# Performance work log

Hardware: AMD Instinct MI355X
Metric: run time of the kernel (lower is better)

The kernel has to match this reference:

```python
import jax, jax.numpy as jnp
import numpy as np
from jax import lax

B, S, F = 64, 63, 64          # batch, window length, num_past_features
T, NF, OUT = 12, 63, 1        # pred_sequence_length, forecast feats, output_size
C, K = 32, 3                  # hidden channels, kernel size
DILS = (1, 2, 4, 8, 16)       # S = (K-1)*sum(DILS)+1 = 63 -> conv stack reduces to length 1


def setup_inputs() -> dict:
    key = jax.random.key(0)
    ks = jax.random.split(key, 8)
    sc = 0.1
    x = jax.random.normal(ks[0], (B, S, F), dtype=jnp.float32)
    x_forecasts = jax.random.normal(ks[1], (B, T, NF), dtype=jnp.float32)
    # per-feature conv stacks stored as grouped-conv weights (feature_group_count=F)
    w0 = jax.random.normal(ks[2], (F * C, 1, K), dtype=jnp.float32) * sc
    b0 = jnp.zeros((F * C,), dtype=jnp.float32)
    wmid = jax.random.normal(ks[3], (3, F * C, C, K), dtype=jnp.float32) * sc
    bmid = jnp.zeros((3, F * C), dtype=jnp.float32)
    wlast = jax.random.normal(ks[4], (F * 1, C, K), dtype=jnp.float32) * sc
    blast = jnp.zeros((F,), dtype=jnp.float32)
    linW = jax.random.normal(ks[5], (OUT, F + NF), dtype=jnp.float32) * sc
    linb = jnp.zeros((OUT,), dtype=jnp.float32)
    return dict(x=x, x_forecasts=x_forecasts, w0=w0, b0=b0, wmid=wmid,
                bmid=bmid, wlast=wlast, blast=blast, linW=linW, linb=linb)


def _dconv(h, w, d):
    # h: [B, F*Cin, L]; grouped dilated conv, one group per past feature
    return lax.conv_general_dilated(h, w, window_strides=(1,), padding='VALID',
                                    rhs_dilation=(d,),
                                    dimension_numbers=('NCH', 'OIH', 'NCH'),
                                    feature_group_count=F)


def _step(xw, xf, w0, b0, wmid, bmid, wlast, blast, linW, linb):
    # xw: [B, S, F] window; xf: [B, NF] forecast features for this step
    h = jnp.transpose(xw, (0, 2, 1))                       # [B, F, S]
    h = jax.nn.relu(_dconv(h, w0, DILS[0]) + b0[None, :, None])
    for k in range(3):
        h = jax.nn.relu(_dconv(h, wmid[k], DILS[k + 1]) + bmid[k][None, :, None])
    h = _dconv(h, wlast, DILS[4]) + blast[None, :, None]   # [B, F, 1], no final relu
    feat = jnp.concatenate([h[:, :, 0], xf], axis=1)       # [B, F+NF]
    return feat @ linW.T + linb                            # [B, OUT]


def reference(x, x_forecasts, w0, b0, wmid, bmid, wlast, blast, linW, linb):
    params = (w0, b0, wmid, bmid, wlast, blast, linW, linb)
    out0 = _step(x, x_forecasts[:, 0], *params)

    def body(carry, xs):
        xw, prev = carry
        xf_i, xf_ip1 = xs
        add = jnp.concatenate([xf_i, prev], axis=1)[:, None, :]   # [B,1,F] since NF+OUT=F
        xw = jnp.concatenate([xw[:, 1:, :], add], axis=1)          # slide window
        out = _step(xw, xf_ip1, *params)
        return (xw, out), out

    xs = (jnp.swapaxes(x_forecasts[:, :-1], 0, 1),   # [T-1, B, NF]
          jnp.swapaxes(x_forecasts[:, 1:], 0, 1))
    _, outs = lax.scan(body, (x, out0), xs)          # [T-1, B, OUT]
    return jnp.swapaxes(jnp.concatenate([out0[None], outs], axis=0), 0, 1)  # [B, T, OUT]
```

## Files before the change

### kernel.cpp

```cpp
#include <hip/hip_runtime.h>


typedef _Float16 f16;
typedef _Float16 h2 __attribute__((ext_vector_type(2)));
typedef _Float16 f16x4 __attribute__((ext_vector_type(4)));
typedef _Float16 f16x8 __attribute__((ext_vector_type(8)));
typedef float f32x16 __attribute__((ext_vector_type(16)));

#define OFF_H4    0
#define OFF_ST    49152
#define ST_L0     0
#define ST_L1     128
#define ST_L2     384
#define ST_L3     896
#define ST_STRIDE 1760
#define OFF_H40   161792
#define OFF_RECH  161856
#define OFF_PRM   166464
#define OFF_XFT   167488

#define RECH_N 9216
#define TAIL_N 59392

#define RPAD 36
#define NROW 100

__device__ __forceinline__ void stage_wrow(
    const float* __restrict__ wmid, int m, int f, int tid, f16* wrow)
{
  const float* src = wmid + m * 196608 + f * 3072 + tid * 12;
  f16* dst = wrow + (tid >> 3) * 100 + (tid & 7) * 12;
#pragma unroll
  for (int u = 0; u < 3; ++u) {
    const float4 v = *reinterpret_cast<const float4*>(src + u * 4);
    dst[u * 4 + 0] = (f16)v.x; dst[u * 4 + 1] = (f16)v.y;
    dst[u * 4 + 2] = (f16)v.z; dst[u * 4 + 3] = (f16)v.w;
  }
}

__device__ __forceinline__ void mfma_tile2(
    const f16* IN, f16* OUT, int d, int base,
    const f16* __restrict__ wrow, int lane, const float* sBias)
{
  const int lg = lane >> 5;
  const int co = lane & 31;
  const int col = base + co;

  f16x8 afr[6];
#pragma unroll
  for (int h = 0; h < 2; ++h) {
    const f16* wp = wrow + co * 100 + (h * 16 + lg * 8) * 3;
    f16x4 w4[6];
#pragma unroll
    for (int u = 0; u < 6; ++u) w4[u] = *(const f16x4*)(wp + u * 4);
#pragma unroll
    for (int t = 0; t < 3; ++t)
#pragma unroll
      for (int j = 0; j < 8; ++j) {
        const int o = 3 * j + t;
        afr[t * 2 + h][j] = w4[o >> 2][o & 3];
      }
  }

  f32x16 acc;
#pragma unroll
  for (int r = 0; r < 16; ++r)
    acc[r] = sBias[(r & 3) + 8 * (r >> 2) + 4 * lg];

#pragma unroll
  for (int t = 0; t < 3; ++t) {
#pragma unroll
    for (int h = 0; h < 2; ++h) {
      const f16* bp = IN + (col + t * d) * RPAD + h * 16 + lg * 8;
      f16x4 lo = *(const f16x4*)bp;
      f16x4 hi = *(const f16x4*)(bp + 4);
      f16x8 b = __builtin_shufflevector(lo, hi, 0, 1, 2, 3, 4, 5, 6, 7);
      acc = __builtin_amdgcn_mfma_f32_32x32x16_f16(afr[t * 2 + h], b, acc, 0, 0, 0);
    }
  }

#pragma unroll
  for (int q = 0; q < 4; ++q) {
    const int co0 = q * 8 + 4 * lg;
    f16x4 w;
#pragma unroll
    for (int e = 0; e < 4; ++e)
      w[e] = (f16)fmaxf(acc[q * 4 + e], 0.f);
    *(f16x4*)(OUT + col * RPAD + co0) = w;
  }
}

__global__ __launch_bounds__(256) void tcn_pre(
    const float* __restrict__ x, const float* __restrict__ xfc,
    const float* __restrict__ w0, const float* __restrict__ b0,
    const float* __restrict__ wmid, const float* __restrict__ bmid,
    const float* __restrict__ wlast, const float* __restrict__ blast,
    const float* __restrict__ linW, const float* __restrict__ linb,
    float* __restrict__ ws)
{
  const int blk = blockIdx.x;
  const int tid = threadIdx.x;

  if (blk >= 4096) {
    const int idx = (blk - 4096) * 256 + tid;
    if (idx < RECH_N) {
      const int e = idx & 7, lane = (idx >> 3) & 63, q = idx >> 9;
      const int i = q * 8 + e;
      const int m = i / 48, r2 = i % 48;
      const int k = r2 >> 4, ci = r2 & 15;
      const int c = lane & 31, cib = (lane >> 5) * 16;
      ((f16*)(ws + OFF_RECH))[idx] =
          (f16)wmid[m * 196608 + (2016 + c) * 96 + (cib + ci) * 3 + k];
    } else if (idx < RECH_N + 1024) {
      const int r = idx - RECH_N;
      const int e = r & 3, lane = (r >> 2) & 63, q = r >> 8;
      const int i = q * 4 + e;
      const int c = lane & 31;
      float v = 0.f;
      if (i < 3)        v = w0[(2016 + c) * 3 + i];
      else if (i == 3)  v = b0[2016 + c];
      else if (i < 7)   v = bmid[(i - 4) * 2048 + 2016 + c];
      else if (i < 10)  v = wlast[63 * 96 + c * 3 + (i - 7)];
      else if (i == 10) v = blast[63];
      else if (i == 11) v = linW[63];
      else if (i == 12) v = linb[0];
      ws[OFF_PRM + r] = v;
    } else if (idx < TAIL_N) {
      const int r = idx - (RECH_N + 1024);
      const int b = r / 768, rem = r % 768;
      const int q = rem >> 8, lane = (rem >> 2) & 63, e = rem & 3;
      const int i = q * 4 + e;
      ws[OFF_XFT + r] = (lane < 63 && i < 12) ? xfc[(b * 12 + i) * 63 + lane] : 0.f;
    }
    return;
  }

  const int b = blk >> 6;
  const int f = blk & 63;
  const bool lastf = (f == 63);
  const int lane = tid & 63;
  const int g = __builtin_amdgcn_readfirstlane(tid >> 6);

  __shared__ float sIn[80];
  __shared__ float sBias[3][32];
  __shared__ f16 actA[NROW * RPAD];
  __shared__ f16 actB[NROW * RPAD];
  __shared__ __align__(8) f16 wrow[32 * 100];

  for (int t = tid; t < 80; t += 256) {
    float v = 0.f;
    if (t < 63)                 v = x[(b * 63 + t) * 64 + f];
    else if (t < 74 && !lastf)  v = xfc[(b * 12 + (t - 63)) * 63 + f];
    sIn[t] = v;
  }
  if (tid < 96) sBias[tid >> 5][tid & 31] = bmid[(tid >> 5) * 2048 + f * 32 + (tid & 31)];
  for (int i = tid; i < (NROW - 72) * RPAD; i += 256) actA[72 * RPAD + i] = (f16)0.f;
  for (int i = tid; i < (NROW - 68) * RPAD; i += 256) actB[68 * RPAD + i] = (f16)0.f;
  stage_wrow(wmid, 0, f, tid, wrow);
  __syncthreads();

  {
    const float* wb  = w0 + (f * 32 + g * 8) * 3;
    const float* bbp = b0 + f * 32 + g * 8;
#pragma unroll
    for (int it = 0; it < 2; ++it) {
      const int p = lane + it * 64;
      if (p < 72) {
        const float i0 = sIn[p], i1 = sIn[p + 1], i2 = sIn[p + 2];
        f16x4 wv[2];
#pragma unroll
        for (int j = 0; j < 8; ++j) {
          float v = fmaf(wb[j * 3 + 0], i0,
                    fmaf(wb[j * 3 + 1], i1,
                    fmaf(wb[j * 3 + 2], i2, bbp[j])));
          wv[j >> 2][j & 3] = (f16)fmaxf(v, 0.f);
        }
        *(f16x4*)(actA + p * RPAD + g * 8)     = wv[0];
        *(f16x4*)(actA + p * RPAD + g * 8 + 4) = wv[1];
      }
    }
  }
  __syncthreads();

  float* st = ws + OFF_ST + b * ST_STRIDE;

  if (lastf) {
    for (int t = tid; t < 128; t += 256)
      st[ST_L0 + t] = (float)actA[(57 + (t >> 5)) * RPAD + (t & 31)];
  }
  if (g < 3) mfma_tile2(actA, actB, 2, g * 32, wrow, lane, sBias[0]);
  __syncthreads();

  stage_wrow(wmid, 1, f, tid, wrow);
  if (lastf) {
    for (int t = tid; t < 256; t += 256)
      st[ST_L1 + t] = (float)actB[(49 + (t >> 5)) * RPAD + (t & 31)];
  }
  __syncthreads();

  if (g < 2) mfma_tile2(actB, actA, 4, g * 32, wrow, lane, sBias[1]);
  __syncthreads();

  stage_wrow(wmid, 2, f, tid, wrow);
  if (lastf) {
    for (int t = tid; t < 512; t += 256)
      st[ST_L2 + t] = (float)actA[(33 + (t >> 5)) * RPAD + (t & 31)];
  }
  __syncthreads();

  if (g < 2) mfma_tile2(actA, actB, 8, g * 32, wrow, lane, sBias[2]);
  __syncthreads();

  if (lastf) {
    for (int t = tid; t < 864; t += 256)
      st[ST_L3 + t] = (float)actB[(1 + (t >> 5)) * RPAD + (t & 31)];
  }
  if (tid < 12) {
    const int p = tid;
    float acc = blast[f];
    const float* wl = wlast + f * 96;
#pragma unroll
    for (int k = 0; k < 3; ++k) {
      const int row = p + 16 * k;
#pragma unroll
      for (int ci0 = 0; ci0 < 32; ci0 += 4) {
        f16x4 av = *(const f16x4*)(actB + row * RPAD + ci0);
#pragma unroll
        for (int e = 0; e < 4; ++e)
          acc = fmaf(wl[(ci0 + e) * 3 + k], (float)av[e], acc);
      }
    }
    if (!lastf) {
      ws[OFF_H4 + b * 768 + (p >> 2) * 256 + f * 4 + (p & 3)] = acc;
    } else {
      ws[OFF_H4 + b * 768 + (p >> 2) * 256 + 63 * 4 + (p & 3)] = 0.f;
      if (p == 0) ws[OFF_H40 + b] = acc;
    }
  }
}


__device__ __forceinline__ float fd2(h2 a, h2 b, float c) {
#if __has_builtin(__builtin_amdgcn_fdot2)
  return __builtin_amdgcn_fdot2(a, b, c, false);
#else
  return fmaf((float)a[0], (float)b[0], fmaf((float)a[1], (float)b[1], c));
#endif
}

__device__ __forceinline__ float dotv(f16x8 w, f16x8 a, float acc) {
  h2 w0 = {w[0], w[1]}, a0 = {a[0], a[1]};
  h2 w1 = {w[2], w[3]}, a1 = {a[2], a[3]};
  h2 w2 = {w[4], w[5]}, a2 = {a[4], a[5]};
  h2 w3 = {w[6], w[7]}, a3 = {a[6], a[7]};
  acc = fd2(w0, a0, acc);
  acc = fd2(w1, a1, acc);
  acc = fd2(w2, a2, acc);
  acc = fd2(w3, a3, acc);
  return acc;
}

__device__ __forceinline__ f16x8 combineh(f16x8 lo, f16x8 hi) {
  f16x8 s = lo + hi;
#pragma unroll
  for (int i = 0; i < 8; ++i) s[i] = (s[i] > (f16)0.f) ? s[i] : (f16)0.f;
  return s;
}

__device__ __forceinline__ void load16f(const float* p, float* r) {
  const float4* q = reinterpret_cast<const float4*>(p);
  const float4 v0 = q[0], v1 = q[1], v2 = q[2], v3 = q[3];
  r[0]=v0.x;  r[1]=v0.y;  r[2]=v0.z;  r[3]=v0.w;
  r[4]=v1.x;  r[5]=v1.y;  r[6]=v1.z;  r[7]=v1.w;
  r[8]=v2.x;  r[9]=v2.y;  r[10]=v2.z; r[11]=v2.w;
  r[12]=v3.x; r[13]=v3.y; r[14]=v3.z; r[15]=v3.w;
}

__global__ __launch_bounds__(64, 1) void tcn_seq(
    const float* __restrict__ x,
    const float* __restrict__ linW,
    const float* __restrict__ ws, float* __restrict__ out)
{
  const int b = blockIdx.x;
  const int tid = threadIdx.x;
  const int c = tid & 31;
  const int h = tid >> 5;
  const int cib = h * 16;

  __shared__ __align__(16) f16 L0h[15 * 32];
  __shared__ __align__(16) f16 L1p[2][19 * 32];
  __shared__ __align__(16) f16 L2p[2][27 * 32];
  __shared__ __align__(16) f16 wseqh[18 * 64 * 8];
  __shared__ __align__(16) float qs[32];
  __shared__ float preArr[12];

  const float* stp = ws + OFF_ST + b * ST_STRIDE;

  for (int t = tid; t < 128; t += 64) L0h[t] = (f16)stp[ST_L0 + t];
  for (int t = tid; t < 256; t += 64) { L1p[0][t] = (f16)stp[ST_L1 + t]; L1p[1][t] = (f16)0.f; }
  for (int t = tid; t < 512; t += 64) { L2p[0][t] = (f16)stp[ST_L2 + t]; L2p[1][t] = (f16)0.f; }

  {
    const f16* rech = (const f16*)(ws + OFF_RECH);
#pragma unroll
    for (int q = 0; q < 18; ++q)
      *(f16x8*)(wseqh + (q * 64 + tid) * 8) = *(const f16x8*)(rech + (q * 64 + tid) * 8);
  }

  float prm[16];
  {
    const float* tab = ws + OFF_PRM;
#pragma unroll
    for (int q = 0; q < 4; ++q) {
      const float4 v = *reinterpret_cast<const float4*>(tab + (q * 64 + tid) * 4);
      prm[q * 4 + 0] = v.x; prm[q * 4 + 1] = v.y;
      prm[q * 4 + 2] = v.z; prm[q * 4 + 3] = v.w;
    }
  }
  const float w00 = prm[0],  w01 = prm[1],  w02 = prm[2],  b00 = prm[3];
  const float bm0 = prm[4],  bm1 = prm[5],  bm2 = prm[6];
  const float wl0c = prm[7], wl1c = prm[8], wl2c = prm[9];
  const float bl = prm[10],  lw63 = prm[11], lb0 = prm[12];

  const float xv61 = x[(b * 63 + 61) * 64 + 63];
  const float xv62 = x[(b * 63 + 62) * 64 + 63];
  const float h40v = ws[OFF_H40 + b];

  float accv[12];
  {
    float lw = 0.f, lwx = 0.f;
    if (tid < 63) { lw = linW[tid]; lwx = linW[64 + tid]; }
    float h4v[12], xv[12];
#pragma unroll
    for (int q = 0; q < 3; ++q) {
      const float4 hv  = *reinterpret_cast<const float4*>(ws + OFF_H4 + b * 768 + q * 256 + tid * 4);
      const float4 xvv = *reinterpret_cast<const float4*>(ws + OFF_XFT + b * 768 + q * 256 + tid * 4);
      h4v[q*4+0] = hv.x; h4v[q*4+1] = hv.y; h4v[q*4+2] = hv.z; h4v[q*4+3] = hv.w;
      xv[q*4+0] = xvv.x; xv[q*4+1] = xvv.y; xv[q*4+2] = xvv.z; xv[q*4+3] = xvv.w;
    }
#pragma unroll
    for (int i = 0; i < 12; ++i) accv[i] = fmaf(lw, h4v[i], lwx * xv[i]);

    if (tid < 32) {
#pragma unroll
      for (int i = 1; i < 12; ++i) {
        const float qc = fmaf(wl0c, stp[ST_L3 + (i - 1) * 32 + tid],
                              wl1c * stp[ST_L3 + (i + 15) * 32 + tid]);
        accv[i] = fmaf(lw63, qc, accv[i]);
      }
    }
#pragma unroll
    for (int r = 1; r < 64; r <<= 1) {
#pragma unroll
      for (int i = 0; i < 12; ++i) accv[i] += __shfl_xor(accv[i], r);
    }
  }
  if (tid == 0) {
#pragma unroll
    for (int i = 1; i < 12; ++i) preArr[i] = accv[i] + lb0 + lw63 * bl;
  }
  __syncthreads();

  const f16* wbase = wseqh;
  asm volatile("" : "+v"(wbase));

  const float out0 = fmaf(lw63, h40v, accv[0] + lb0);
  if (tid == 0) out[b * 12 + 0] = out0;
  float o1 = out0, o2 = xv62, o3 = xv61;

#pragma unroll 1
  for (int s = 1; s < 12; ++s) {
    const float preS = preArr[s];

    const float nL0 = fmaxf(fmaf(w00, o3, fmaf(w01, o2, fmaf(w02, o1, b00))), 0.f);
    L0h[(3 + s) * 32 + c] = (f16)nL0;

    float v1;
    {
      const f16* wp = wbase + (0 * 6 * 64 + tid) * 8;
      f16x8 W0 = *(const f16x8*)(wp);
      f16x8 W1 = *(const f16x8*)(wp + 64 * 8);
      f16x8 W2 = *(const f16x8*)(wp + 2 * 64 * 8);
      f16x8 W3 = *(const f16x8*)(wp + 3 * 64 * 8);
      f16x8 W4 = *(const f16x8*)(wp + 4 * 64 * 8);
      f16x8 W5 = *(const f16x8*)(wp + 5 * 64 * 8);
      const f16* r0p = L0h + (s - 1) * 32 + cib;
      const f16* r1p = L0h + (s + 1) * 32 + cib;
      const f16* np  = L0h + (3 + s) * 32 + cib;
      f16x8 R0a = *(const f16x8*)r0p, R0b = *(const f16x8*)(r0p + 8);
      f16x8 R1a = *(const f16x8*)r1p, R1b = *(const f16x8*)(r1p + 8);
      f16x8 Na  = *(const f16x8*)np,  Nb  = *(const f16x8*)(np + 8);
      float a0 = dotv(W0, R0a, 0.f), a1 = dotv(W1, R0b, 0.f);
      a0 = dotv(W2, R1a, a0);        a1 = dotv(W3, R1b, a1);
      a0 = dotv(W4, Na, a0);         a1 = dotv(W5, Nb, a1);
      v1 = a0 + a1 + (h == 0 ? bm0 : 0.f);
    }
    L1p[h][(7 + s) * 32 + c] = (f16)v1;

    float v2;
    {
      const f16* wp = wbase + (1 * 6 * 64 + tid) * 8;
      f16x8 W0 = *(const f16x8*)(wp);
      f16x8 W1 = *(const f16x8*)(wp + 64 * 8);
      f16x8 W2 = *(const f16x8*)(wp + 2 * 64 * 8);
      f16x8 W3 = *(const f16x8*)(wp + 3 * 64 * 8);
      f16x8 W4 = *(const f16x8*)(wp + 4 * 64 * 8);
      f16x8 W5 = *(const f16x8*)(wp + 5 * 64 * 8);
      const int i0 = (s - 1) * 32 + cib, i1 = (s + 3) * 32 + cib, in = (7 + s) * 32 + cib;
      f16x8 R0a = combineh(*(const f16x8*)(&L1p[0][i0]),     *(const f16x8*)(&L1p[1][i0]));
      f16x8 R0b = combineh(*(const f16x8*)(&L1p[0][i0 + 8]), *(const f16x8*)(&L1p[1][i0 + 8]));
      f16x8 R1a = combineh(*(const f16x8*)(&L1p[0][i1]),     *(const f16x8*)(&L1p[1][i1]));
      f16x8 R1b = combineh(*(const f16x8*)(&L1p[0][i1 + 8]), *(const f16x8*)(&L1p[1][i1 + 8]));
      f16x8 Na  = combineh(*(const f16x8*)(&L1p[0][in]),     *(const f16x8*)(&L1p[1][in]));
      f16x8 Nb  = combineh(*(const f16x8*)(&L1p[0][in + 8]), *(const f16x8*)(&L1p[1][in + 8]));
      float a0 = dotv(W0, R0a, 0.f), a1 = dotv(W1, R0b, 0.f);
      a0 = dotv(W2, R1a, a0);        a1 = dotv(W3, R1b, a1);
      a0 = dotv(W4, Na, a0);         a1 = dotv(W5, Nb, a1);
      v2 = a0 + a1 + (h == 0 ? bm1 : 0.f);
    }
    L2p[h][(15 + s) * 32 + c] = (f16)v2;

    float v3;
    {
      const f16* wp = wbase + (2 * 6 * 64 + tid) * 8;
      f16x8 W0 = *(const f16x8*)(wp);
      f16x8 W1 = *(const f16x8*)(wp + 64 * 8);
      f16x8 W2 = *(const f16x8*)(wp + 2 * 64 * 8);
      f16x8 W3 = *(const f16x8*)(wp + 3 * 64 * 8);
      f16x8 W4 = *(const f16x8*)(wp + 4 * 64 * 8);
      f16x8 W5 = *(const f16x8*)(wp + 5 * 64 * 8);
      const int i0 = (s - 1) * 32 + cib, i1 = (s + 7) * 32 + cib, in = (15 + s) * 32 + cib;
      f16x8 R0a = combineh(*(const f16x8*)(&L2p[0][i0]),     *(const f16x8*)(&L2p[1][i0]));
      f16x8 R0b = combineh(*(const f16x8*)(&L2p[0][i0 + 8]), *(const f16x8*)(&L2p[1][i0 + 8]));
      f16x8 R1a = combineh(*(const f16x8*)(&L2p[0][i1]),     *(const f16x8*)(&L2p[1][i1]));
      f16x8 R1b = combineh(*(const f16x8*)(&L2p[0][i1 + 8]), *(const f16x8*)(&L2p[1][i1 + 8]));
      f16x8 Na  = combineh(*(const f16x8*)(&L2p[0][in]),     *(const f16x8*)(&L2p[1][in]));
      f16x8 Nb  = combineh(*(const f16x8*)(&L2p[0][in + 8]), *(const f16x8*)(&L2p[1][in + 8]));
      float a0 = dotv(W0, R0a, 0.f), a1 = dotv(W1, R0b, 0.f);
      a0 = dotv(W2, R1a, a0);        a1 = dotv(W3, R1b, a1);
      a0 = dotv(W4, Na, a0);         a1 = dotv(W5, Nb, a1);
      v3 = a0 + a1 + (h == 0 ? bm2 : 0.f);
    }
    v3 += __shfl_xor(v3, 32);
    const float nL3 = fmaxf(v3, 0.f);

    if (h == 0) qs[c] = wl2c * nL3;
    float qa[16], qb[16];
    load16f(qs, qa); load16f(qs + 16, qb);
    float s0 = 0.f, s1 = 0.f, s2 = 0.f, s3 = 0.f;
#pragma unroll
    for (int i = 0; i < 16; i += 4) {
      s0 += qa[i + 0] + qb[i + 0];
      s1 += qa[i + 1] + qb[i + 1];
      s2 += qa[i + 2] + qb[i + 2];
      s3 += qa[i + 3] + qb[i + 3];
    }
    const float S = (s0 + s1) + (s2 + s3);
    const float outs = fmaf(lw63, S, preS);
    if (tid == 0) out[b * 12 + s] = outs;
    o3 = o2; o2 = o1; o1 = outs;
  }
}


extern "C" void kernel_launch(void* const* d_in, const int* in_sizes, int n_in,
                              void* d_out, int out_size, void* d_ws, size_t ws_size,
                              hipStream_t stream) {
  const float* x     = (const float*)d_in[0];
  const float* xfc   = (const float*)d_in[1];
  const float* w0    = (const float*)d_in[2];
  const float* b0    = (const float*)d_in[3];
  const float* wmid  = (const float*)d_in[4];
  const float* bmid  = (const float*)d_in[5];
  const float* wlast = (const float*)d_in[6];
  const float* blast = (const float*)d_in[7];
  const float* linW  = (const float*)d_in[8];
  const float* linb  = (const float*)d_in[9];
  float* out = (float*)d_out;
  float* ws  = (float*)d_ws;

  tcn_pre<<<4096 + 232, 256, 0, stream>>>(
      x, xfc, w0, b0, wmid, bmid, wlast, blast, linW, linb, ws);
  tcn_seq<<<64, 64, 0, stream>>>(x, linW, ws, out);
}
```

Baseline: 41.85 us.

## Fuse pre and sequential kernels into one launch with atomic-counter handoff

Merges the parallel conv-stack kernel and the per-batch sequential kernel into a single launch. The trailing 64 blocks spin on global atomic counters until all compute and tail-prep blocks have finished, then run the recurrent steps. They also prefetch the reshaped weights as soon as the tail counter completes. This removes one kernel launch and the gap between launches, but adds a memset and relies on all earlier blocks being scheduled before the spinning blocks, which risks deadlock if they are not.

```diff
diff --git a/kernel.cpp b/kernel.cpp
--- a/kernel.cpp
+++ b/kernel.cpp
@@ -18,12 +18,24 @@
 #define OFF_RECH  161856
 #define OFF_PRM   166464
 #define OFF_XFT   167488
+#define OFF_CTR   216640
 
 #define RECH_N 9216
 #define TAIL_N 59392
+#define NCOMP  4096
+#define NTAIL  232
+#define NSEQ   64
 
 #define RPAD 36
 #define NROW 100
+
+#if __has_builtin(__builtin_amdgcn_fence)
+#define ACQ_FENCE() __builtin_amdgcn_fence(__ATOMIC_ACQUIRE, "agent")
+#else
+#define ACQ_FENCE() __threadfence()
+#endif
+
+#define SMEM_BYTES 25472
 
 __device__ __forceinline__ void stage_wrow(
     const float* __restrict__ wmid, int m, int f, int tid, f16* wrow)
@@ -90,19 +102,250 @@
   }
 }
 
-__global__ __launch_bounds__(256) void tcn_pre(
+__device__ __forceinline__ float fd2(h2 a, h2 b, float c) {
+#if __has_builtin(__builtin_amdgcn_fdot2)
+  return __builtin_amdgcn_fdot2(a, b, c, false);
+#else
+  return fmaf((float)a[0], (float)b[0], fmaf((float)a[1], (float)b[1], c));
+#endif
+}
+
+__device__ __forceinline__ float dotv(f16x8 w, f16x8 a, float acc) {
+  h2 w0 = {w[0], w[1]}, a0 = {a[0], a[1]};
+  h2 w1 = {w[2], w[3]}, a1 = {a[2], a[3]};
+  h2 w2 = {w[4], w[5]}, a2 = {a[4], a[5]};
+  h2 w3 = {w[6], w[7]}, a3 = {a[6], a[7]};
+  acc = fd2(w0, a0, acc);
+  acc = fd2(w1, a1, acc);
+  acc = fd2(w2, a2, acc);
+  acc = fd2(w3, a3, acc);
+  return acc;
+}
+
+__device__ __forceinline__ f16x8 combineh(f16x8 lo, f16x8 hi) {
+  f16x8 s = lo + hi;
+#pragma unroll
+  for (int i = 0; i < 8; ++i) s[i] = (s[i] > (f16)0.f) ? s[i] : (f16)0.f;
+  return s;
+}
+
+__device__ __forceinline__ void load16f(const float* p, float* r) {
+  const float4* q = reinterpret_cast<const float4*>(p);
+  const float4 v0 = q[0], v1 = q[1], v2 = q[2], v3 = q[3];
+  r[0]=v0.x;  r[1]=v0.y;  r[2]=v0.z;  r[3]=v0.w;
+  r[4]=v1.x;  r[5]=v1.y;  r[6]=v1.z;  r[7]=v1.w;
+  r[8]=v2.x;  r[9]=v2.y;  r[10]=v2.z; r[11]=v2.w;
+  r[12]=v3.x; r[13]=v3.y; r[14]=v3.z; r[15]=v3.w;
+}
+
+__global__ __launch_bounds__(256) void tcn_all(
     const float* __restrict__ x, const float* __restrict__ xfc,
     const float* __restrict__ w0, const float* __restrict__ b0,
     const float* __restrict__ wmid, const float* __restrict__ bmid,
     const float* __restrict__ wlast, const float* __restrict__ blast,
     const float* __restrict__ linW, const float* __restrict__ linb,
-    float* __restrict__ ws)
+    float* __restrict__ ws, float* __restrict__ out)
 {
+  __shared__ __align__(16) char smem[SMEM_BYTES];
   const int blk = blockIdx.x;
   const int tid = threadIdx.x;
-
-  if (blk >= 4096) {
-    const int idx = (blk - 4096) * 256 + tid;
+  int* ctr = (int*)(ws + OFF_CTR);
+
+  if (blk >= NCOMP + NTAIL) {
+    if (tid >= 64) return;
+    const int b = blk - (NCOMP + NTAIL);
+    const int c = tid & 31;
+    const int h = tid >> 5;
+    const int cib = h * 16;
+
+    f16* wseqh = (f16*)smem;
+    f16* L0h   = (f16*)(smem + 18432);
+    f16* L1p0  = (f16*)(smem + 19392);
+    f16* L1p1  = (f16*)(smem + 20608);
+    f16* L2p0  = (f16*)(smem + 21824);
+    f16* L2p1  = (f16*)(smem + 23552);
+    float* qs     = (float*)(smem + 25280);
+    float* preArr = (float*)(smem + 25408);
+
+    const float xv61 = x[(b * 63 + 61) * 64 + 63];
+    const float xv62 = x[(b * 63 + 62) * 64 + 63];
+    float lw = 0.f, lwx = 0.f;
+    if (tid < 63) { lw = linW[tid]; lwx = linW[64 + tid]; }
+
+    while (__hip_atomic_load(&ctr[1], __ATOMIC_RELAXED, __HIP_MEMORY_SCOPE_AGENT) < NTAIL)
+      __builtin_amdgcn_s_sleep(4);
+    ACQ_FENCE();
+
+    {
+      const f16* rech = (const f16*)(ws + OFF_RECH);
+#pragma unroll
+      for (int q = 0; q < 18; ++q)
+        *(f16x8*)(wseqh + (q * 64 + tid) * 8) = *(const f16x8*)(rech + (q * 64 + tid) * 8);
+    }
+    float prm[16];
+    {
+      const float* tab = ws + OFF_PRM;
+#pragma unroll
+      for (int q = 0; q < 4; ++q) {
+        const float4 v = *reinterpret_cast<const float4*>(tab + (q * 64 + tid) * 4);
+        prm[q * 4 + 0] = v.x; prm[q * 4 + 1] = v.y;
+        prm[q * 4 + 2] = v.z; prm[q * 4 + 3] = v.w;
+      }
+    }
+    float xv[12];
+#pragma unroll
+    for (int q = 0; q < 3; ++q) {
+      const float4 vv = *reinterpret_cast<const float4*>(ws + OFF_XFT + b * 768 + q * 256 + tid * 4);
+      xv[q*4+0] = vv.x; xv[q*4+1] = vv.y; xv[q*4+2] = vv.z; xv[q*4+3] = vv.w;
+    }
+    const float w00 = prm[0],  w01 = prm[1],  w02 = prm[2],  b00 = prm[3];
+    const float bm0 = prm[4],  bm1 = prm[5],  bm2 = prm[6];
+    const float wl0c = prm[7], wl1c = prm[8], wl2c = prm[9];
+    const float bl = prm[10],  lw63 = prm[11], lb0 = prm[12];
+
+    while (__hip_atomic_load(&ctr[0], __ATOMIC_RELAXED, __HIP_MEMORY_SCOPE_AGENT) < NCOMP)
+      __builtin_amdgcn_s_sleep(4);
+    ACQ_FENCE();
+
+    const float* stp = ws + OFF_ST + b * ST_STRIDE;
+    for (int t = tid; t < 128; t += 64) L0h[t] = (f16)stp[ST_L0 + t];
+    for (int t = tid; t < 256; t += 64) { L1p0[t] = (f16)stp[ST_L1 + t]; L1p1[t] = (f16)0.f; }
+    for (int t = tid; t < 512; t += 64) { L2p0[t] = (f16)stp[ST_L2 + t]; L2p1[t] = (f16)0.f; }
+    const float h40v = ws[OFF_H40 + b];
+
+    float accv[12];
+    {
+      float h4v[12];
+#pragma unroll
+      for (int q = 0; q < 3; ++q) {
+        const float4 hv = *reinterpret_cast<const float4*>(ws + OFF_H4 + b * 768 + q * 256 + tid * 4);
+        h4v[q*4+0] = hv.x; h4v[q*4+1] = hv.y; h4v[q*4+2] = hv.z; h4v[q*4+3] = hv.w;
+      }
+#pragma unroll
+      for (int i = 0; i < 12; ++i) accv[i] = fmaf(lw, h4v[i], lwx * xv[i]);
+      if (tid < 32) {
+#pragma unroll
+        for (int i = 1; i < 12; ++i) {
+          const float qc = fmaf(wl0c, stp[ST_L3 + (i - 1) * 32 + tid],
+                                wl1c * stp[ST_L3 + (i + 15) * 32 + tid]);
+          accv[i] = fmaf(lw63, qc, accv[i]);
+        }
+      }
+#pragma unroll
+      for (int r = 1; r < 64; r <<= 1) {
+#pragma unroll
+        for (int i = 0; i < 12; ++i) accv[i] += __shfl_xor(accv[i], r);
+      }
+    }
+    if (tid == 0) {
+#pragma unroll
+      for (int i = 1; i < 12; ++i) preArr[i] = accv[i] + lb0 + lw63 * bl;
+    }
+
+    const f16* wbase = wseqh;
+    asm volatile("" : "+v"(wbase));
+
+    const float out0 = fmaf(lw63, h40v, accv[0] + lb0);
+    if (tid == 0) out[b * 12 + 0] = out0;
+    float o1 = out0, o2 = xv62, o3 = xv61;
+
+#pragma unroll 1
+    for (int s = 1; s < 12; ++s) {
+      const float preS = preArr[s];
+
+      const float nL0 = fmaxf(fmaf(w00, o3, fmaf(w01, o2, fmaf(w02, o1, b00))), 0.f);
+      L0h[(3 + s) * 32 + c] = (f16)nL0;
+
+      float v1;
+      {
+        const f16* wp = wbase + (0 * 6 * 64 + tid) * 8;
+        f16x8 W0 = *(const f16x8*)(wp);
+        f16x8 W1 = *(const f16x8*)(wp + 64 * 8);
+        f16x8 W2 = *(const f16x8*)(wp + 2 * 64 * 8);
+        f16x8 W3 = *(const f16x8*)(wp + 3 * 64 * 8);
+        f16x8 W4 = *(const f16x8*)(wp + 4 * 64 * 8);
+        f16x8 W5 = *(const f16x8*)(wp + 5 * 64 * 8);
+        const f16* r0p = L0h + (s - 1) * 32 + cib;
+        const f16* r1p = L0h + (s + 1) * 32 + cib;
+        const f16* np  = L0h + (3 + s) * 32 + cib;
+        f16x8 R0a = *(const f16x8*)r0p, R0b = *(const f16x8*)(r0p + 8);
+        f16x8 R1a = *(const f16x8*)r1p, R1b = *(const f16x8*)(r1p + 8);
+        f16x8 Na  = *(const f16x8*)np,  Nb  = *(const f16x8*)(np + 8);
+        float a0 = dotv(W0, R0a, 0.f), a1 = dotv(W1, R0b, 0.f);
+        a0 = dotv(W2, R1a, a0);        a1 = dotv(W3, R1b, a1);
+        a0 = dotv(W4, Na, a0);         a1 = dotv(W5, Nb, a1);
+        v1 = a0 + a1 + (h == 0 ? bm0 : 0.f);
+      }
+      (h ? L1p1 : L1p0)[(7 + s) * 32 + c] = (f16)v1;
+
+      float v2;
+      {
+        const f16* wp = wbase + (1 * 6 * 64 + tid) * 8;
+        f16x8 W0 = *(const f16x8*)(wp);
+        f16x8 W1 = *(const f16x8*)(wp + 64 * 8);
+        f16x8 W2 = *(const f16x8*)(wp + 2 * 64 * 8);
+        f16x8 W3 = *(const f16x8*)(wp + 3 * 64 * 8);
+        f16x8 W4 = *(const f16x8*)(wp + 4 * 64 * 8);
+        f16x8 W5 = *(const f16x8*)(wp + 5 * 64 * 8);
+        const int i0 = (s - 1) * 32 + cib, i1 = (s + 3) * 32 + cib, in = (7 + s) * 32 + cib;
+        f16x8 R0a = combineh(*(const f16x8*)(L1p0 + i0),     *(const f16x8*)(L1p1 + i0));
+        f16x8 R0b = combineh(*(const f16x8*)(L1p0 + i0 + 8), *(const f16x8*)(L1p1 + i0 + 8));
+        f16x8 R1a = combineh(*(const f16x8*)(L1p0 + i1),     *(const f16x8*)(L1p1 + i1));
+        f16x8 R1b = combineh(*(const f16x8*)(L1p0 + i1 + 8), *(const f16x8*)(L1p1 + i1 + 8));
+        f16x8 Na  = combineh(*(const f16x8*)(L1p0 + in),     *(const f16x8*)(L1p1 + in));
+        f16x8 Nb  = combineh(*(const f16x8*)(L1p0 + in + 8), *(const f16x8*)(L1p1 + in + 8));
+        float a0 = dotv(W0, R0a, 0.f), a1 = dotv(W1, R0b, 0.f);
+        a0 = dotv(W2, R1a, a0);        a1 = dotv(W3, R1b, a1);
+        a0 = dotv(W4, Na, a0);         a1 = dotv(W5, Nb, a1);
+        v2 = a0 + a1 + (h == 0 ? bm1 : 0.f);
+      }
+      (h ? L2p1 : L2p0)[(15 + s) * 32 + c] = (f16)v2;
+
+      float v3;
+      {
+        const f16* wp = wbase + (2 * 6 * 64 + tid) * 8;
+        f16x8 W0 = *(const f16x8*)(wp);
+        f16x8 W1 = *(const f16x8*)(wp + 64 * 8);
+        f16x8 W2 = *(const f16x8*)(wp + 2 * 64 * 8);
+        f16x8 W3 = *(const f16x8*)(wp + 3 * 64 * 8);
+        f16x8 W4 = *(const f16x8*)(wp + 4 * 64 * 8);
+        f16x8 W5 = *(const f16x8*)(wp + 5 * 64 * 8);
+        const int i0 = (s - 1) * 32 + cib, i1 = (s + 7) * 32 + cib, in = (15 + s) * 32 + cib;
+        f16x8 R0a = combineh(*(const f16x8*)(L2p0 + i0),     *(const f16x8*)(L2p1 + i0));
+        f16x8 R0b = combineh(*(const f16x8*)(L2p0 + i0 + 8), *(const f16x8*)(L2p1 + i0 + 8));
+        f16x8 R1a = combineh(*(const f16x8*)(L2p0 + i1),     *(const f16x8*)(L2p1 + i1));
+        f16x8 R1b = combineh(*(const f16x8*)(L2p0 + i1 + 8), *(const f16x8*)(L2p1 + i1 + 8));
+        f16x8 Na  = combineh(*(const f16x8*)(L2p0 + in),     *(const f16x8*)(L2p1 + in));
+        f16x8 Nb  = combineh(*(const f16x8*)(L2p0 + in + 8), *(const f16x8*)(L2p1 + in + 8));
+        float a0 = dotv(W0, R0a, 0.f), a1 = dotv(W1, R0b, 0.f);
+        a0 = dotv(W2, R1a, a0);        a1 = dotv(W3, R1b, a1);
+        a0 = dotv(W4, Na, a0);         a1 = dotv(W5, Nb, a1);
+        v3 = a0 + a1 + (h == 0 ? bm2 : 0.f);
+      }
+      v3 += __shfl_xor(v3, 32);
+      const float nL3 = fmaxf(v3, 0.f);
+
+      if (h == 0) qs[c] = wl2c * nL3;
+      float qa[16], qb[16];
+      load16f(qs, qa); load16f(qs + 16, qb);
+      float s0 = 0.f, s1 = 0.f, s2 = 0.f, s3 = 0.f;
+#pragma unroll
+      for (int i = 0; i < 16; i += 4) {
+        s0 += qa[i + 0] + qb[i + 0];
+        s1 += qa[i + 1] + qb[i + 1];
+        s2 += qa[i + 2] + qb[i + 2];
+        s3 += qa[i + 3] + qb[i + 3];
+      }
+      const float S = (s0 + s1) + (s2 + s3);
+      const float outs = fmaf(lw63, S, preS);
+      if (tid == 0) out[b * 12 + s] = outs;
+      o3 = o2; o2 = o1; o1 = outs;
+    }
+    return;
+  }
+
+  if (blk >= NCOMP) {
+    const int idx = (blk - NCOMP) * 256 + tid;
     if (idx < RECH_N) {
       const int e = idx & 7, lane = (idx >> 3) & 63, q = idx >> 9;
       const int i = q * 8 + e;
@@ -125,13 +368,15 @@
       else if (i == 11) v = linW[63];
       else if (i == 12) v = linb[0];
       ws[OFF_PRM + r] = v;
-    } else if (idx < TAIL_N) {
+    } else {
       const int r = idx - (RECH_N + 1024);
       const int b = r / 768, rem = r % 768;
       const int q = rem >> 8, lane = (rem >> 2) & 63, e = rem & 3;
       const int i = q * 4 + e;
       ws[OFF_XFT + r] = (lane < 63 && i < 12) ? xfc[(b * 12 + i) * 63 + lane] : 0.f;
     }
+    __syncthreads();
+    if (tid == 0) { __threadfence(); atomicAdd(&ctr[1], 1); }
     return;
   }
 
@@ -141,11 +386,11 @@
   const int lane = tid & 63;
   const int g = __builtin_amdgcn_readfirstlane(tid >> 6);
 
-  __shared__ float sIn[80];
-  __shared__ float sBias[3][32];
-  __shared__ f16 actA[NROW * RPAD];
-  __shared__ f16 actB[NROW * RPAD];
-  __shared__ __align__(8) f16 wrow[32 * 100];
+  float* sIn   = (float*)smem;
+  float* sBias = (float*)(smem + 320);
+  f16*   actA  = (f16*)(smem + 704);
+  f16*   actB  = (f16*)(smem + 7904);
+  f16*   wrow  = (f16*)(smem + 15104);
 
   for (int t = tid; t < 80; t += 256) {
     float v = 0.f;
@@ -153,7 +398,7 @@
     else if (t < 74 && !lastf)  v = xfc[(b * 12 + (t - 63)) * 63 + f];
     sIn[t] = v;
   }
-  if (tid < 96) sBias[tid >> 5][tid & 31] = bmid[(tid >> 5) * 2048 + f * 32 + (tid & 31)];
+  if (tid < 96) sBias[(tid >> 5) * 32 + (tid & 31)] = bmid[(tid >> 5) * 2048 + f * 32 + (tid & 31)];
   for (int i = tid; i < (NROW - 72) * RPAD; i += 256) actA[72 * RPAD + i] = (f16)0.f;
   for (int i = tid; i < (NROW - 68) * RPAD; i += 256) actB[68 * RPAD + i] = (f16)0.f;
   stage_wrow(wmid, 0, f, tid, wrow);
@@ -188,7 +433,7 @@
     for (int t = tid; t < 128; t += 256)
       st[ST_L0 + t] = (float)actA[(57 + (t >> 5)) * RPAD + (t & 31)];
   }
-  if (g < 3) mfma_tile2(actA, actB, 2, g * 32, wrow, lane, sBias[0]);
+  if (g < 3) mfma_tile2(actA, actB, 2, g * 32, wrow, lane, sBias + 0);
   __syncthreads();
 
   stage_wrow(wmid, 1, f, tid, wrow);
@@ -198,7 +443,7 @@
   }
   __syncthreads();
 
-  if (g < 2) mfma_tile2(actB, actA, 4, g * 32, wrow, lane, sBias[1]);
+  if (g < 2) mfma_tile2(actB, actA, 4, g * 32, wrow, lane, sBias + 32);
   __syncthreads();
 
   stage_wrow(wmid, 2, f, tid, wrow);
@@ -208,7 +453,7 @@
   }
   __syncthreads();
 
-  if (g < 2) mfma_tile2(actA, actB, 8, g * 32, wrow, lane, sBias[2]);
+  if (g < 2) mfma_tile2(actA, actB, 8, g * 32, wrow, lane, sBias + 64);
   __syncthreads();
 
   if (lastf) {
@@ -237,229 +482,8 @@
       if (p == 0) ws[OFF_H40 + b] = acc;
     }
   }
-}
-
-
-__device__ __forceinline__ float fd2(h2 a, h2 b, float c) {
-#if __has_builtin(__builtin_amdgcn_fdot2)
-  return __builtin_amdgcn_fdot2(a, b, c, false);
-#else
-  return fmaf((float)a[0], (float)b[0], fmaf((float)a[1], (float)b[1], c));
-#endif
-}
-
-__device__ __forceinline__ float dotv(f16x8 w, f16x8 a, float acc) {
-  h2 w0 = {w[0], w[1]}, a0 = {a[0], a[1]};
-  h2 w1 = {w[2], w[3]}, a1 = {a[2], a[3]};
-  h2 w2 = {w[4], w[5]}, a2 = {a[4], a[5]};
-  h2 w3 = {w[6], w[7]}, a3 = {a[6], a[7]};
-  acc = fd2(w0, a0, acc);
-  acc = fd2(w1, a1, acc);
-  acc = fd2(w2, a2, acc);
-  acc = fd2(w3, a3, acc);
-  return acc;
-}
-
-__device__ __forceinline__ f16x8 combineh(f16x8 lo, f16x8 hi) {
-  f16x8 s = lo + hi;
-#pragma unroll
-  for (int i = 0; i < 8; ++i) s[i] = (s[i] > (f16)0.f) ? s[i] : (f16)0.f;
-  return s;
-}
-
-__device__ __forceinline__ void load16f(const float* p, float* r) {
-  const float4* q = reinterpret_cast<const float4*>(p);
-  const float4 v0 = q[0], v1 = q[1], v2 = q[2], v3 = q[3];
-  r[0]=v0.x;  r[1]=v0.y;  r[2]=v0.z;  r[3]=v0.w;
-  r[4]=v1.x;  r[5]=v1.y;  r[6]=v1.z;  r[7]=v1.w;
-  r[8]=v2.x;  r[9]=v2.y;  r[10]=v2.z; r[11]=v2.w;
-  r[12]=v3.x; r[13]=v3.y; r[14]=v3.z; r[15]=v3.w;
-}
-
-__global__ __launch_bounds__(64, 1) void tcn_seq(
-    const float* __restrict__ x,
-    const float* __restrict__ linW,
-    const float* __restrict__ ws, float* __restrict__ out)
-{
-  const int b = blockIdx.x;
-  const int tid = threadIdx.x;
-  const int c = tid & 31;
-  const int h = tid >> 5;
-  const int cib = h * 16;
-
-  __shared__ __align__(16) f16 L0h[15 * 32];
-  __shared__ __align__(16) f16 L1p[2][19 * 32];
-  __shared__ __align__(16) f16 L2p[2][27 * 32];
-  __shared__ __align__(16) f16 wseqh[18 * 64 * 8];
-  __shared__ __align__(16) float qs[32];
-  __shared__ float preArr[12];
-
-  const float* stp = ws + OFF_ST + b * ST_STRIDE;
-
-  for (int t = tid; t < 128; t += 64) L0h[t] = (f16)stp[ST_L0 + t];
-  for (int t = tid; t < 256; t += 64) { L1p[0][t] = (f16)stp[ST_L1 + t]; L1p[1][t] = (f16)0.f; }
-  for (int t = tid; t < 512; t += 64) { L2p[0][t] = (f16)stp[ST_L2 + t]; L2p[1][t] = (f16)0.f; }
-
-  {
-    const f16* rech = (const f16*)(ws + OFF_RECH);
-#pragma unroll
-    for (int q = 0; q < 18; ++q)
-      *(f16x8*)(wseqh + (q * 64 + tid) * 8) = *(const f16x8*)(rech + (q * 64 + tid) * 8);
-  }
-
-  float prm[16];
-  {
-    const float* tab = ws + OFF_PRM;
-#pragma unroll
-    for (int q = 0; q < 4; ++q) {
-      const float4 v = *reinterpret_cast<const float4*>(tab + (q * 64 + tid) * 4);
-      prm[q * 4 + 0] = v.x; prm[q * 4 + 1] = v.y;
-      prm[q * 4 + 2] = v.z; prm[q * 4 + 3] = v.w;
-    }
-  }
-  const float w00 = prm[0],  w01 = prm[1],  w02 = prm[2],  b00 = prm[3];
-  const float bm0 = prm[4],  bm1 = prm[5],  bm2 = prm[6];
-  const float wl0c = prm[7], wl1c = prm[8], wl2c = prm[9];
-  const float bl = prm[10],  lw63 = prm[11], lb0 = prm[12];
-
-  const float xv61 = x[(b * 63 + 61) * 64 + 63];
-  const float xv62 = x[(b * 63 + 62) * 64 + 63];
-  const float h40v = ws[OFF_H40 + b];
-
-  float accv[12];
-  {
-    float lw = 0.f, lwx = 0.f;
-    if (tid < 63) { lw = linW[tid]; lwx = linW[64 + tid]; }
-    float h4v[12], xv[12];
-#pragma unroll
-    for (int q = 0; q < 3; ++q) {
-      const float4 hv  = *reinterpret_cast<const float4*>(ws + OFF_H4 + b * 768 + q * 256 + tid * 4);
-      const float4 xvv = *reinterpret_cast<const float4*>(ws + OFF_XFT + b * 768 + q * 256 + tid * 4);
-      h4v[q*4+0] = hv.x; h4v[q*4+1] = hv.y; h4v[q*4+2] = hv.z; h4v[q*4+3] = hv.w;
-      xv[q*4+0] = xvv.x; xv[q*4+1] = xvv.y; xv[q*4+2] = xvv.z; xv[q*4+3] = xvv.w;
-    }
-#pragma unroll
-    for (int i = 0; i < 12; ++i) accv[i] = fmaf(lw, h4v[i], lwx * xv[i]);
-
-    if (tid < 32) {
-#pragma unroll
-      for (int i = 1; i < 12; ++i) {
-        const float qc = fmaf(wl0c, stp[ST_L3 + (i - 1) * 32 + tid],
-                              wl1c * stp[ST_L3 + (i + 15) * 32 + tid]);
-        accv[i] = fmaf(lw63, qc, accv[i]);
-      }
-    }
-#pragma unroll
-    for (int r = 1; r < 64; r <<= 1) {
-#pragma unroll
-      for (int i = 0; i < 12; ++i) accv[i] += __shfl_xor(accv[i], r);
-    }
-  }
-  if (tid == 0) {
-#pragma unroll
-    for (int i = 1; i < 12; ++i) preArr[i] = accv[i] + lb0 + lw63 * bl;
-  }
-  __syncthreads();
-
-  const f16* wbase = wseqh;
-  asm volatile("" : "+v"(wbase));
-
-  const float out0 = fmaf(lw63, h40v, accv[0] + lb0);
-  if (tid == 0) out[b * 12 + 0] = out0;
-  float o1 = out0, o2 = xv62, o3 = xv61;
-
-#pragma unroll 1
-  for (int s = 1; s < 12; ++s) {
-    const float preS = preArr[s];
-
-    const float nL0 = fmaxf(fmaf(w00, o3, fmaf(w01, o2, fmaf(w02, o1, b00))), 0.f);
-    L0h[(3 + s) * 32 + c] = (f16)nL0;
-
-    float v1;
-    {
-      const f16* wp = wbase + (0 * 6 * 64 + tid) * 8;
-      f16x8 W0 = *(const f16x8*)(wp);
-      f16x8 W1 = *(const f16x8*)(wp + 64 * 8);
-      f16x8 W2 = *(const f16x8*)(wp + 2 * 64 * 8);
-      f16x8 W3 = *(const f16x8*)(wp + 3 * 64 * 8);
-      f16x8 W4 = *(const f16x8*)(wp + 4 * 64 * 8);
-      f16x8 W5 = *(const f16x8*)(wp + 5 * 64 * 8);
-      const f16* r0p = L0h + (s - 1) * 32 + cib;
-      const f16* r1p = L0h + (s + 1) * 32 + cib;
-      const f16* np  = L0h + (3 + s) * 32 + cib;
-      f16x8 R0a = *(const f16x8*)r0p, R0b = *(const f16x8*)(r0p + 8);
-      f16x8 R1a = *(const f16x8*)r1p, R1b = *(const f16x8*)(r1p + 8);
-      f16x8 Na  = *(const f16x8*)np,  Nb  = *(const f16x8*)(np + 8);
-      float a0 = dotv(W0, R0a, 0.f), a1 = dotv(W1, R0b, 0.f);
-      a0 = dotv(W2, R1a, a0);        a1 = dotv(W3, R1b, a1);
-      a0 = dotv(W4, Na, a0);         a1 = dotv(W5, Nb, a1);
-      v1 = a0 + a1 + (h == 0 ? bm0 : 0.f);
-    }
-    L1p[h][(7 + s) * 32 + c] = (f16)v1;
-
-    float v2;
-    {
-      const f16* wp = wbase + (1 * 6 * 64 + tid) * 8;
-      f16x8 W0 = *(const f16x8*)(wp);
-      f16x8 W1 = *(const f16x8*)(wp + 64 * 8);
-      f16x8 W2 = *(const f16x8*)(wp + 2 * 64 * 8);
-      f16x8 W3 = *(const f16x8*)(wp + 3 * 64 * 8);
-      f16x8 W4 = *(const f16x8*)(wp + 4 * 64 * 8);
-      f16x8 W5 = *(const f16x8*)(wp + 5 * 64 * 8);
-      const int i0 = (s - 1) * 32 + cib, i1 = (s + 3) * 32 + cib, in = (7 + s) * 32 + cib;
-      f16x8 R0a = combineh(*(const f16x8*)(&L1p[0][i0]),     *(const f16x8*)(&L1p[1][i0]));
-      f16x8 R0b = combineh(*(const f16x8*)(&L1p[0][i0 + 8]), *(const f16x8*)(&L1p[1][i0 + 8]));
-      f16x8 R1a = combineh(*(const f16x8*)(&L1p[0][i1]),     *(const f16x8*)(&L1p[1][i1]));
-      f16x8 R1b = combineh(*(const f16x8*)(&L1p[0][i1 + 8]), *(const f16x8*)(&L1p[1][i1 + 8]));
-      f16x8 Na  = combineh(*(const f16x8*)(&L1p[0][in]),     *(const f16x8*)(&L1p[1][in]));
-      f16x8 Nb  = combineh(*(const f16x8*)(&L1p[0][in + 8]), *(const f16x8*)(&L1p[1][in + 8]));
-      float a0 = dotv(W0, R0a, 0.f), a1 = dotv(W1, R0b, 0.f);
-      a0 = dotv(W2, R1a, a0);        a1 = dotv(W3, R1b, a1);
-      a0 = dotv(W4, Na, a0);         a1 = dotv(W5, Nb, a1);
-      v2 = a0 + a1 + (h == 0 ? bm1 : 0.f);
-    }
-    L2p[h][(15 + s) * 32 + c] = (f16)v2;
-
-    float v3;
-    {
-      const f16* wp = wbase + (2 * 6 * 64 + tid) * 8;
-      f16x8 W0 = *(const f16x8*)(wp);
-      f16x8 W1 = *(const f16x8*)(wp + 64 * 8);
-      f16x8 W2 = *(const f16x8*)(wp + 2 * 64 * 8);
-      f16x8 W3 = *(const f16x8*)(wp + 3 * 64 * 8);
-      f16x8 W4 = *(const f16x8*)(wp + 4 * 64 * 8);
-      f16x8 W5 = *(const f16x8*)(wp + 5 * 64 * 8);
-      const int i0 = (s - 1) * 32 + cib, i1 = (s + 7) * 32 + cib, in = (15 + s) * 32 + cib;
-      f16x8 R0a = combineh(*(const f16x8*)(&L2p[0][i0]),     *(const f16x8*)(&L2p[1][i0]));
-      f16x8 R0b = combineh(*(const f16x8*)(&L2p[0][i0 + 8]), *(const f16x8*)(&L2p[1][i0 + 8]));
-      f16x8 R1a = combineh(*(const f16x8*)(&L2p[0][i1]),     *(const f16x8*)(&L2p[1][i1]));
-      f16x8 R1b = combineh(*(const f16x8*)(&L2p[0][i1 + 8]), *(const f16x8*)(&L2p[1][i1 + 8]));
-      f16x8 Na  = combineh(*(const f16x8*)(&L2p[0][in]),     *(const f16x8*)(&L2p[1][in]));
-      f16x8 Nb  = combineh(*(const f16x8*)(&L2p[0][in + 8]), *(const f16x8*)(&L2p[1][in + 8]));
-      float a0 = dotv(W0, R0a, 0.f), a1 = dotv(W1, R0b, 0.f);
-      a0 = dotv(W2, R1a, a0);        a1 = dotv(W3, R1b, a1);
-      a0 = dotv(W4, Na, a0);         a1 = dotv(W5, Nb, a1);
-      v3 = a0 + a1 + (h == 0 ? bm2 : 0.f);
-    }
-    v3 += __shfl_xor(v3, 32);
-    const float nL3 = fmaxf(v3, 0.f);
-
-    if (h == 0) qs[c] = wl2c * nL3;
-    float qa[16], qb[16];
-    load16f(qs, qa); load16f(qs + 16, qb);
-    float s0 = 0.f, s1 = 0.f, s2 = 0.f, s3 = 0.f;
-#pragma unroll
-    for (int i = 0; i < 16; i += 4) {
-      s0 += qa[i + 0] + qb[i + 0];
-      s1 += qa[i + 1] + qb[i + 1];
-      s2 += qa[i + 2] + qb[i + 2];
-      s3 += qa[i + 3] + qb[i + 3];
-    }
-    const float S = (s0 + s1) + (s2 + s3);
-    const float outs = fmaf(lw63, S, preS);
-    if (tid == 0) out[b * 12 + s] = outs;
-    o3 = o2; o2 = o1; o1 = outs;
-  }
+  __syncthreads();
+  if (tid == 0) { __threadfence(); atomicAdd(&ctr[0], 1); }
 }
 
 
@@ -479,7 +503,7 @@
   float* out = (float*)d_out;
   float* ws  = (float*)d_ws;
 
-  tcn_pre<<<4096 + 232, 256, 0, stream>>>(
-      x, xfc, w0, b0, wmid, bmid, wlast, blast, linW, linb, ws);
-  tcn_seq<<<64, 64, 0, stream>>>(x, linW, ws, out);
-}
+  hipMemsetAsync((char*)d_ws + OFF_CTR * sizeof(float), 0, 8, stream);
+  tcn_all<<<NCOMP + NTAIL + NSEQ, 256, 0, stream>>>(
+      x, xfc, w0, b0, wmid, bmid, wlast, blast, linW, linb, ws, out);
+}
```

New measurement: 152.0 us. +263.2%, slower.
